# Kernel optimization log

Measured on AMD Instinct MI355X. Metric: run time of the kernel, lower is better.

## Reference

```python
import jax, jax.numpy as jnp
import numpy as np

T, TOPK = 512, 2
E, H, D = 8, 2816, 1024


def setup_inputs() -> dict:
    key = jax.random.key(0)
    k1, k2, k3, k4, k5 = jax.random.split(key, 5)
    x = jax.random.normal(k1, (T, D), dtype=jnp.float32)
    expert_indices = jax.random.randint(k2, (T, TOPK), 0, E, dtype=jnp.int64)
    w1 = jax.random.normal(k3, (E, H, D), dtype=jnp.float32)
    w2 = jax.random.normal(k4, (E, H, D), dtype=jnp.float32)
    w3 = jax.random.normal(k5, (E, H, D), dtype=jnp.float32)
    return {"x": x, "expert_indices": expert_indices, "w1": w1, "w2": w2, "w3": w3}


def reference(x, expert_indices, w1, w2, w3):
    # Math identical to: silu(x @ w1[e].T) * (x @ w3[e].T) @ w2[e] for e = expert_indices[t, a].
    # Computed densely over all experts (GEMM-friendly), then gathered per token,
    # which avoids materializing [T, a, H, D] gathered weight tensors.
    h1 = jax.nn.silu(jnp.einsum('ti,ehi->teh', x, w1))   # [T, E, H]
    h3 = jnp.einsum('ti,ehi->teh', x, w3)                # [T, E, H]
    out_all = jnp.einsum('teh,ehi->tei', h1 * h3, w2)    # [T, E, D]
    # gather the top_k selected experts per token -> [T, TOPK, D]
    idx = expert_indices[:, :, None]                     # [T, a, 1]
    expert_outs = jnp.take_along_axis(out_all, idx, axis=1)
    return expert_outs
```

## Files before the change

kernel.cpp:

```cpp
#include <hip/hip_runtime.h>


#define NEXP 8
#define HDIM 2816
#define DDIM 1024
#define NPAIR 1024

typedef unsigned int uint;
typedef unsigned short ushort;
typedef __attribute__((ext_vector_type(8))) short bf16x8;
typedef __attribute__((ext_vector_type(4))) float fvec4;
typedef __attribute__((ext_vector_type(4))) uint uvec4;
typedef __attribute__((ext_vector_type(2))) uint uvec2;

__device__ __forceinline__ ushort f2bf(float f) {
    uint u = __builtin_bit_cast(uint, f);
    u += 0x7fff + ((u >> 16) & 1);
    return (ushort)(u >> 16);
}
__device__ __forceinline__ uint pack2(float lo, float hi) {
    return (uint)f2bf(lo) | ((uint)f2bf(hi) << 16);
}

__global__ void route_kernel(const int* __restrict__ idx,
                             int* __restrict__ counts,
                             int* __restrict__ lists) {
    int p = threadIdx.x;
    if (p < NEXP) counts[p] = 0;
    __syncthreads();
    int e = idx[p];
    int pos = atomicAdd(&counts[e], 1);
    lists[e * NPAIR + pos] = p;
}

__global__ void h_mfma(const float* __restrict__ x,
                       const float* __restrict__ w1,
                       const float* __restrict__ w3,
                       const int* __restrict__ counts,
                       const int* __restrict__ lists,
                       ushort* __restrict__ hb) {
    const int e = blockIdx.x;
    const int cnt = counts[e];
    const int m0 = blockIdx.z * 128;
    if (m0 >= cnt) return;
    const int h0 = blockIdx.y * 64;

    __shared__ ushort sA[128 * 32];
    __shared__ ushort sB1[64 * 32];
    __shared__ ushort sB3[64 * 32];
    __shared__ int sTok[128];
    __shared__ int sPairS[128];

    const int tid = threadIdx.x;
    if (tid < 128) {
        int m = m0 + tid;
        int mc = (m < cnt) ? m : (cnt - 1);
        int p = lists[e * NPAIR + mc];
        sTok[tid] = p >> 1;
        sPairS[tid] = (m < cnt) ? p : -1;
    }
    __syncthreads();

    const int w = tid >> 6;
    const int lane = tid & 63;
    const int l16 = lane & 15;
    const int quad = lane >> 4;

    fvec4 acc1[2][4], acc3[2][4];
    #pragma unroll
    for (int i = 0; i < 2; ++i)
        #pragma unroll
        for (int j = 0; j < 4; ++j) { acc1[i][j] = (fvec4)0.f; acc3[i][j] = (fvec4)0.f; }

    const float* w1e = w1 + (size_t)e * HDIM * DDIM + (size_t)h0 * DDIM;
    const float* w3e = w3 + (size_t)e * HDIM * DDIM + (size_t)h0 * DDIM;

    for (int k0 = 0; k0 < DDIM; k0 += 32) {
        fvec4 va[4], vb1[2], vb3[2];
        #pragma unroll
        for (int it = 0; it < 4; ++it) {
            int ii = tid + it * 256;
            int row = ii >> 3, c4 = ii & 7;
            va[it] = *(const fvec4*)(x + (size_t)sTok[row] * DDIM + k0 + c4 * 4);
        }
        #pragma unroll
        for (int it = 0; it < 2; ++it) {
            int ii = tid + it * 256;
            int row = ii >> 3, c4 = ii & 7;
            vb1[it] = *(const fvec4*)(w1e + (size_t)row * DDIM + k0 + c4 * 4);
            vb3[it] = *(const fvec4*)(w3e + (size_t)row * DDIM + k0 + c4 * 4);
        }
        __syncthreads();
        #pragma unroll
        for (int it = 0; it < 4; ++it) {
            int ii = tid + it * 256;
            int row = ii >> 3, c4 = ii & 7;
            uvec2 t = { pack2(va[it][0], va[it][1]), pack2(va[it][2], va[it][3]) };
            *(uvec2*)&sA[row * 32 + c4 * 4] = t;
        }
        #pragma unroll
        for (int it = 0; it < 2; ++it) {
            int ii = tid + it * 256;
            int row = ii >> 3, c4 = ii & 7;
            uvec2 t1 = { pack2(vb1[it][0], vb1[it][1]), pack2(vb1[it][2], vb1[it][3]) };
            uvec2 t3 = { pack2(vb3[it][0], vb3[it][1]), pack2(vb3[it][2], vb3[it][3]) };
            *(uvec2*)&sB1[row * 32 + c4 * 4] = t1;
            *(uvec2*)&sB3[row * 32 + c4 * 4] = t3;
        }
        __syncthreads();

        bf16x8 bf1[4], bf3[4];
        #pragma unroll
        for (int ni = 0; ni < 4; ++ni) {
            bf1[ni] = *(const bf16x8*)&sB1[(ni * 16 + l16) * 32 + quad * 8];
            bf3[ni] = *(const bf16x8*)&sB3[(ni * 16 + l16) * 32 + quad * 8];
        }
        #pragma unroll
        for (int mi = 0; mi < 2; ++mi) {
            bf16x8 af = *(const bf16x8*)&sA[(w * 32 + mi * 16 + l16) * 32 + quad * 8];
            #pragma unroll
            for (int ni = 0; ni < 4; ++ni) {
                acc1[mi][ni] = __builtin_amdgcn_mfma_f32_16x16x32_bf16(af, bf1[ni], acc1[mi][ni], 0, 0, 0);
                acc3[mi][ni] = __builtin_amdgcn_mfma_f32_16x16x32_bf16(af, bf3[ni], acc3[mi][ni], 0, 0, 0);
            }
        }
    }

    #pragma unroll
    for (int mi = 0; mi < 2; ++mi)
        #pragma unroll
        for (int r = 0; r < 4; ++r) {
            int m = w * 32 + mi * 16 + quad * 4 + r;
            int p = sPairS[m];
            if (p >= 0) {
                size_t base = (size_t)p * HDIM + h0;
                #pragma unroll
                for (int ni = 0; ni < 4; ++ni) {
                    float a = acc1[mi][ni][r];
                    float g = acc3[mi][ni][r];
                    float s = a / (1.f + __expf(-a)) * g;
                    hb[base + ni * 16 + l16] = f2bf(s);
                }
            }
        }
}

__global__ void out_mfma(const float* __restrict__ w2,
                         const int* __restrict__ counts,
                         const int* __restrict__ lists,
                         const ushort* __restrict__ hb,
                         float* __restrict__ out) {
    const int e = blockIdx.x;
    const int cnt = counts[e];
    const int m0 = blockIdx.z * 128;
    if (m0 >= cnt) return;
    const int n0 = blockIdx.y * 32;

    __shared__ ushort sA[128 * 64];
    __shared__ ushort sB[32 * 64];
    __shared__ int sPairC[128];
    __shared__ int sPairS[128];

    const int tid = threadIdx.x;
    if (tid < 128) {
        int m = m0 + tid;
        int mc = (m < cnt) ? m : (cnt - 1);
        int p = lists[e * NPAIR + mc];
        sPairC[tid] = p;
        sPairS[tid] = (m < cnt) ? p : -1;
    }
    __syncthreads();

    const int w = tid >> 6;
    const int lane = tid & 63;
    const int l16 = lane & 15;
    const int quad = lane >> 4;

    fvec4 acc[2][2];
    #pragma unroll
    for (int i = 0; i < 2; ++i) { acc[i][0] = (fvec4)0.f; acc[i][1] = (fvec4)0.f; }

    const float* w2e = w2 + (size_t)e * HDIM * DDIM + n0;
    const int kp = tid >> 3;
    const int n4 = tid & 7;

    for (int k0 = 0; k0 < HDIM; k0 += 64) {
        uvec4 va[4];
        #pragma unroll
        for (int it = 0; it < 4; ++it) {
            int ii = tid + it * 256;
            int row = ii >> 3, c = ii & 7;
            va[it] = *(const uvec4*)(hb + (size_t)sPairC[row] * HDIM + k0 + c * 8);
        }
        fvec4 fa = *(const fvec4*)(w2e + (size_t)(k0 + kp * 2) * DDIM + n4 * 4);
        fvec4 fb = *(const fvec4*)(w2e + (size_t)(k0 + kp * 2 + 1) * DDIM + n4 * 4);
        __syncthreads();
        #pragma unroll
        for (int it = 0; it < 4; ++it) {
            int ii = tid + it * 256;
            int row = ii >> 3, c = ii & 7;
            *(uvec4*)&sA[row * 64 + c * 8] = va[it];
        }
        #pragma unroll
        for (int j = 0; j < 4; ++j) {
            int n = n4 * 4 + j;
            *(uint*)&sB[n * 64 + kp * 2] = pack2(fa[j], fb[j]);
        }
        __syncthreads();

        #pragma unroll
        for (int kk = 0; kk < 64; kk += 32) {
            bf16x8 bfr[2];
            #pragma unroll
            for (int ni = 0; ni < 2; ++ni)
                bfr[ni] = *(const bf16x8*)&sB[(ni * 16 + l16) * 64 + kk + quad * 8];
            #pragma unroll
            for (int mi = 0; mi < 2; ++mi) {
                bf16x8 af = *(const bf16x8*)&sA[(w * 32 + mi * 16 + l16) * 64 + kk + quad * 8];
                #pragma unroll
                for (int ni = 0; ni < 2; ++ni)
                    acc[mi][ni] = __builtin_amdgcn_mfma_f32_16x16x32_bf16(af, bfr[ni], acc[mi][ni], 0, 0, 0);
            }
        }
    }

    #pragma unroll
    for (int mi = 0; mi < 2; ++mi)
        #pragma unroll
        for (int r = 0; r < 4; ++r) {
            int m = w * 32 + mi * 16 + quad * 4 + r;
            int p = sPairS[m];
            if (p >= 0) {
                #pragma unroll
                for (int ni = 0; ni < 2; ++ni)
                    out[(size_t)p * DDIM + n0 + ni * 16 + l16] = acc[mi][ni][r];
            }
        }
}

extern "C" void kernel_launch(void* const* d_in, const int* in_sizes, int n_in,
                              void* d_out, int out_size, void* d_ws, size_t ws_size,
                              hipStream_t stream) {
    const float* x   = (const float*)d_in[0];
    const int*   idx = (const int*)d_in[1];
    const float* w1  = (const float*)d_in[2];
    const float* w2  = (const float*)d_in[3];
    const float* w3  = (const float*)d_in[4];
    float* out = (float*)d_out;

    char* ws = (char*)d_ws;
    int*    counts = (int*)ws;
    int*    lists  = (int*)(ws + 1024);
    ushort* hbuf   = (ushort*)(ws + 65536);

    route_kernel<<<1, NPAIR, 0, stream>>>(idx, counts, lists);
    h_mfma<<<dim3(NEXP, HDIM / 64, NPAIR / 128), 256, 0, stream>>>(
        x, w1, w3, counts, lists, hbuf);
    out_mfma<<<dim3(NEXP, DDIM / 32, NPAIR / 128), 256, 0, stream>>>(
        w2, counts, lists, hbuf, out);
}
```

Measured before the change: 325.3 us.

## Prefetch next K tile, pad LDS, use 512-thread blocks and split-K atomics

Both GEMM kernels now run 512 threads per block, each wave owning 16 rows, and load the next K-chunk from global memory into registers while MFMAs run on the current LDS tile. LDS rows are padded (36/68 halfwords) to reduce bank conflicts. The output GEMM widens the N tile to 64 and splits K four ways, accumulating into a zeroed output with float atomicAdd. This adds parallelism and overlap, at the cost of a memset, atomic traffic and nondeterministic summation order.

New measurement: 320.3 us. Within noise of the previous version (-1.5%).

```diff
diff --git a/kernel.cpp b/kernel.cpp
--- a/kernel.cpp
+++ b/kernel.cpp
@@ -22,9 +22,9 @@
     return (uint)f2bf(lo) | ((uint)f2bf(hi) << 16);
 }
 
-__global__ void route_kernel(const int* __restrict__ idx,
-                             int* __restrict__ counts,
-                             int* __restrict__ lists) {
+__global__ __launch_bounds__(1024) void route_kernel(const int* __restrict__ idx,
+                                                     int* __restrict__ counts,
+                                                     int* __restrict__ lists) {
     int p = threadIdx.x;
     if (p < NEXP) counts[p] = 0;
     __syncthreads();
@@ -33,7 +33,9 @@
     lists[e * NPAIR + pos] = p;
 }
 
-__global__ void h_mfma(const float* __restrict__ x,
+#define LDA1 36
+
+__global__ __launch_bounds__(512) void h_mfma(const float* __restrict__ x,
                        const float* __restrict__ w1,
                        const float* __restrict__ w3,
                        const int* __restrict__ counts,
@@ -45,9 +47,9 @@
     if (m0 >= cnt) return;
     const int h0 = blockIdx.y * 64;
 
-    __shared__ ushort sA[128 * 32];
-    __shared__ ushort sB1[64 * 32];
-    __shared__ ushort sB3[64 * 32];
+    __shared__ ushort sA[128 * LDA1];
+    __shared__ ushort sB1[64 * LDA1];
+    __shared__ ushort sB3[64 * LDA1];
     __shared__ int sTok[128];
     __shared__ int sPairS[128];
 
@@ -66,98 +68,92 @@
     const int l16 = lane & 15;
     const int quad = lane >> 4;
 
-    fvec4 acc1[2][4], acc3[2][4];
-    #pragma unroll
-    for (int i = 0; i < 2; ++i)
-        #pragma unroll
-        for (int j = 0; j < 4; ++j) { acc1[i][j] = (fvec4)0.f; acc3[i][j] = (fvec4)0.f; }
+    const int arow = tid >> 3;
+    const int ac4  = tid & 7;
+
+    fvec4 acc1[4], acc3[4];
+    #pragma unroll
+    for (int i = 0; i < 4; ++i) { acc1[i] = (fvec4)0.f; acc3[i] = (fvec4)0.f; }
 
     const float* w1e = w1 + (size_t)e * HDIM * DDIM + (size_t)h0 * DDIM;
     const float* w3e = w3 + (size_t)e * HDIM * DDIM + (size_t)h0 * DDIM;
+    const float* xr0 = x + (size_t)sTok[arow] * DDIM + ac4 * 4;
+    const float* xr1 = x + (size_t)sTok[arow + 64] * DDIM + ac4 * 4;
+    const float* wr1 = w1e + (size_t)arow * DDIM + ac4 * 4;
+    const float* wr3 = w3e + (size_t)arow * DDIM + ac4 * 4;
+
+    fvec4 va0, va1, vb1, vb3;
+    va0 = *(const fvec4*)(xr0);
+    va1 = *(const fvec4*)(xr1);
+    vb1 = *(const fvec4*)(wr1);
+    vb3 = *(const fvec4*)(wr3);
 
     for (int k0 = 0; k0 < DDIM; k0 += 32) {
-        fvec4 va[4], vb1[2], vb3[2];
-        #pragma unroll
-        for (int it = 0; it < 4; ++it) {
-            int ii = tid + it * 256;
-            int row = ii >> 3, c4 = ii & 7;
-            va[it] = *(const fvec4*)(x + (size_t)sTok[row] * DDIM + k0 + c4 * 4);
-        }
-        #pragma unroll
-        for (int it = 0; it < 2; ++it) {
-            int ii = tid + it * 256;
-            int row = ii >> 3, c4 = ii & 7;
-            vb1[it] = *(const fvec4*)(w1e + (size_t)row * DDIM + k0 + c4 * 4);
-            vb3[it] = *(const fvec4*)(w3e + (size_t)row * DDIM + k0 + c4 * 4);
-        }
-        __syncthreads();
-        #pragma unroll
-        for (int it = 0; it < 4; ++it) {
-            int ii = tid + it * 256;
-            int row = ii >> 3, c4 = ii & 7;
-            uvec2 t = { pack2(va[it][0], va[it][1]), pack2(va[it][2], va[it][3]) };
-            *(uvec2*)&sA[row * 32 + c4 * 4] = t;
-        }
-        #pragma unroll
-        for (int it = 0; it < 2; ++it) {
-            int ii = tid + it * 256;
-            int row = ii >> 3, c4 = ii & 7;
-            uvec2 t1 = { pack2(vb1[it][0], vb1[it][1]), pack2(vb1[it][2], vb1[it][3]) };
-            uvec2 t3 = { pack2(vb3[it][0], vb3[it][1]), pack2(vb3[it][2], vb3[it][3]) };
-            *(uvec2*)&sB1[row * 32 + c4 * 4] = t1;
-            *(uvec2*)&sB3[row * 32 + c4 * 4] = t3;
-        }
-        __syncthreads();
-
-        bf16x8 bf1[4], bf3[4];
+        __syncthreads();
+        {
+            uvec2 t;
+            t = (uvec2){ pack2(va0[0], va0[1]), pack2(va0[2], va0[3]) };
+            *(uvec2*)&sA[arow * LDA1 + ac4 * 4] = t;
+            t = (uvec2){ pack2(va1[0], va1[1]), pack2(va1[2], va1[3]) };
+            *(uvec2*)&sA[(arow + 64) * LDA1 + ac4 * 4] = t;
+            t = (uvec2){ pack2(vb1[0], vb1[1]), pack2(vb1[2], vb1[3]) };
+            *(uvec2*)&sB1[arow * LDA1 + ac4 * 4] = t;
+            t = (uvec2){ pack2(vb3[0], vb3[1]), pack2(vb3[2], vb3[3]) };
+            *(uvec2*)&sB3[arow * LDA1 + ac4 * 4] = t;
+        }
+        __syncthreads();
+
+        int kn = (k0 + 32 < DDIM) ? (k0 + 32) : k0;
+        va0 = *(const fvec4*)(xr0 + kn);
+        va1 = *(const fvec4*)(xr1 + kn);
+        vb1 = *(const fvec4*)(wr1 + kn);
+        vb3 = *(const fvec4*)(wr3 + kn);
+
+        bf16x8 af = *(const bf16x8*)&sA[(w * 16 + l16) * LDA1 + quad * 8];
         #pragma unroll
         for (int ni = 0; ni < 4; ++ni) {
-            bf1[ni] = *(const bf16x8*)&sB1[(ni * 16 + l16) * 32 + quad * 8];
-            bf3[ni] = *(const bf16x8*)&sB3[(ni * 16 + l16) * 32 + quad * 8];
-        }
-        #pragma unroll
-        for (int mi = 0; mi < 2; ++mi) {
-            bf16x8 af = *(const bf16x8*)&sA[(w * 32 + mi * 16 + l16) * 32 + quad * 8];
+            bf16x8 b1 = *(const bf16x8*)&sB1[(ni * 16 + l16) * LDA1 + quad * 8];
+            bf16x8 b3 = *(const bf16x8*)&sB3[(ni * 16 + l16) * LDA1 + quad * 8];
+            acc1[ni] = __builtin_amdgcn_mfma_f32_16x16x32_bf16(af, b1, acc1[ni], 0, 0, 0);
+            acc3[ni] = __builtin_amdgcn_mfma_f32_16x16x32_bf16(af, b3, acc3[ni], 0, 0, 0);
+        }
+    }
+
+    #pragma unroll
+    for (int r = 0; r < 4; ++r) {
+        int m = w * 16 + quad * 4 + r;
+        int p = sPairS[m];
+        if (p >= 0) {
+            size_t base = (size_t)p * HDIM + h0;
             #pragma unroll
             for (int ni = 0; ni < 4; ++ni) {
-                acc1[mi][ni] = __builtin_amdgcn_mfma_f32_16x16x32_bf16(af, bf1[ni], acc1[mi][ni], 0, 0, 0);
-                acc3[mi][ni] = __builtin_amdgcn_mfma_f32_16x16x32_bf16(af, bf3[ni], acc3[mi][ni], 0, 0, 0);
+                float a = acc1[ni][r];
+                float g = acc3[ni][r];
+                float s = a / (1.f + __expf(-a)) * g;
+                hb[base + ni * 16 + l16] = f2bf(s);
             }
         }
     }
-
-    #pragma unroll
-    for (int mi = 0; mi < 2; ++mi)
-        #pragma unroll
-        for (int r = 0; r < 4; ++r) {
-            int m = w * 32 + mi * 16 + quad * 4 + r;
-            int p = sPairS[m];
-            if (p >= 0) {
-                size_t base = (size_t)p * HDIM + h0;
-                #pragma unroll
-                for (int ni = 0; ni < 4; ++ni) {
-                    float a = acc1[mi][ni][r];
-                    float g = acc3[mi][ni][r];
-                    float s = a / (1.f + __expf(-a)) * g;
-                    hb[base + ni * 16 + l16] = f2bf(s);
-                }
-            }
-        }
-}
-
-__global__ void out_mfma(const float* __restrict__ w2,
+}
+
+#define LDA2 68
+
+__global__ __launch_bounds__(512) void out_mfma(const float* __restrict__ w2,
                          const int* __restrict__ counts,
                          const int* __restrict__ lists,
                          const ushort* __restrict__ hb,
                          float* __restrict__ out) {
     const int e = blockIdx.x;
     const int cnt = counts[e];
-    const int m0 = blockIdx.z * 128;
+    const int mb = blockIdx.z >> 2;
+    const int sk = blockIdx.z & 3;
+    const int m0 = mb * 128;
     if (m0 >= cnt) return;
-    const int n0 = blockIdx.y * 32;
-
-    __shared__ ushort sA[128 * 64];
-    __shared__ ushort sB[32 * 64];
+    const int n0 = blockIdx.y * 64;
+    const int kbase = sk * (HDIM / 4);
+
+    __shared__ ushort sA[128 * LDA2];
+    __shared__ ushort sB[64 * LDA2];
     __shared__ int sPairC[128];
     __shared__ int sPairS[128];
 
@@ -176,66 +172,65 @@
     const int l16 = lane & 15;
     const int quad = lane >> 4;
 
-    fvec4 acc[2][2];
-    #pragma unroll
-    for (int i = 0; i < 2; ++i) { acc[i][0] = (fvec4)0.f; acc[i][1] = (fvec4)0.f; }
+    const int arow = tid >> 3;
+    const int ac   = tid & 7;
+    const int kp   = tid >> 4;
+    const int n4   = tid & 15;
+
+    fvec4 acc[4];
+    #pragma unroll
+    for (int i = 0; i < 4; ++i) acc[i] = (fvec4)0.f;
 
     const float* w2e = w2 + (size_t)e * HDIM * DDIM + n0;
-    const int kp = tid >> 3;
-    const int n4 = tid & 7;
-
-    for (int k0 = 0; k0 < HDIM; k0 += 64) {
-        uvec4 va[4];
+    const ushort* ha0 = hb + (size_t)sPairC[arow] * HDIM + ac * 8;
+    const ushort* ha1 = hb + (size_t)sPairC[arow + 64] * HDIM + ac * 8;
+    const float* wk0 = w2e + (size_t)(kbase + 2 * kp) * DDIM + n4 * 4;
+
+    uvec4 va0, va1;
+    fvec4 fa, fb;
+    va0 = *(const uvec4*)(ha0 + kbase);
+    va1 = *(const uvec4*)(ha1 + kbase);
+    fa = *(const fvec4*)(wk0);
+    fb = *(const fvec4*)(wk0 + DDIM);
+
+    const int NCH = (HDIM / 4) / 64;
+    for (int kc = 0; kc < NCH; ++kc) {
+        __syncthreads();
+        *(uvec4*)&sA[arow * LDA2 + ac * 8] = va0;
+        *(uvec4*)&sA[(arow + 64) * LDA2 + ac * 8] = va1;
         #pragma unroll
-        for (int it = 0; it < 4; ++it) {
-            int ii = tid + it * 256;
-            int row = ii >> 3, c = ii & 7;
-            va[it] = *(const uvec4*)(hb + (size_t)sPairC[row] * HDIM + k0 + c * 8);
-        }
-        fvec4 fa = *(const fvec4*)(w2e + (size_t)(k0 + kp * 2) * DDIM + n4 * 4);
-        fvec4 fb = *(const fvec4*)(w2e + (size_t)(k0 + kp * 2 + 1) * DDIM + n4 * 4);
-        __syncthreads();
-        #pragma unroll
-        for (int it = 0; it < 4; ++it) {
-            int ii = tid + it * 256;
-            int row = ii >> 3, c = ii & 7;
-            *(uvec4*)&sA[row * 64 + c * 8] = va[it];
-        }
-        #pragma unroll
-        for (int j = 0; j < 4; ++j) {
-            int n = n4 * 4 + j;
-            *(uint*)&sB[n * 64 + kp * 2] = pack2(fa[j], fb[j]);
-        }
-        __syncthreads();
+        for (int j = 0; j < 4; ++j)
+            *(uint*)&sB[(n4 * 4 + j) * LDA2 + kp * 2] = pack2(fa[j], fb[j]);
+        __syncthreads();
+
+        int kcn = (kc + 1 < NCH) ? (kc + 1) : kc;
+        int koff = kcn * 64;
+        va0 = *(const uvec4*)(ha0 + kbase + koff);
+        va1 = *(const uvec4*)(ha1 + kbase + koff);
+        fa = *(const fvec4*)(wk0 + (size_t)koff * DDIM);
+        fb = *(const fvec4*)(wk0 + (size_t)(koff + 1) * DDIM);
 
         #pragma unroll
         for (int kk = 0; kk < 64; kk += 32) {
-            bf16x8 bfr[2];
+            bf16x8 af = *(const bf16x8*)&sA[(w * 16 + l16) * LDA2 + kk + quad * 8];
             #pragma unroll
-            for (int ni = 0; ni < 2; ++ni)
-                bfr[ni] = *(const bf16x8*)&sB[(ni * 16 + l16) * 64 + kk + quad * 8];
+            for (int ni = 0; ni < 4; ++ni) {
+                bf16x8 bf = *(const bf16x8*)&sB[(ni * 16 + l16) * LDA2 + kk + quad * 8];
+                acc[ni] = __builtin_amdgcn_mfma_f32_16x16x32_bf16(af, bf, acc[ni], 0, 0, 0);
+            }
+        }
+    }
+
+    #pragma unroll
+    for (int r = 0; r < 4; ++r) {
+        int m = w * 16 + quad * 4 + r;
+        int p = sPairS[m];
+        if (p >= 0) {
             #pragma unroll
-            for (int mi = 0; mi < 2; ++mi) {
-                bf16x8 af = *(const bf16x8*)&sA[(w * 32 + mi * 16 + l16) * 64 + kk + quad * 8];
-                #pragma unroll
-                for (int ni = 0; ni < 2; ++ni)
-                    acc[mi][ni] = __builtin_amdgcn_mfma_f32_16x16x32_bf16(af, bfr[ni], acc[mi][ni], 0, 0, 0);
-            }
-        }
-    }
-
-    #pragma unroll
-    for (int mi = 0; mi < 2; ++mi)
-        #pragma unroll
-        for (int r = 0; r < 4; ++r) {
-            int m = w * 32 + mi * 16 + quad * 4 + r;
-            int p = sPairS[m];
-            if (p >= 0) {
-                #pragma unroll
-                for (int ni = 0; ni < 2; ++ni)
-                    out[(size_t)p * DDIM + n0 + ni * 16 + l16] = acc[mi][ni][r];
-            }
-        }
+            for (int ni = 0; ni < 4; ++ni)
+                atomicAdd(&out[(size_t)p * DDIM + n0 + ni * 16 + l16], acc[ni][r]);
+        }
+    }
 }
 
 extern "C" void kernel_launch(void* const* d_in, const int* in_sizes, int n_in,
@@ -253,9 +248,10 @@
     int*    lists  = (int*)(ws + 1024);
     ushort* hbuf   = (ushort*)(ws + 65536);
 
+    hipMemsetAsync(out, 0, (size_t)out_size * sizeof(float), stream);
     route_kernel<<<1, NPAIR, 0, stream>>>(idx, counts, lists);
-    h_mfma<<<dim3(NEXP, HDIM / 64, NPAIR / 128), 256, 0, stream>>>(
+    h_mfma<<<dim3(NEXP, HDIM / 64, NPAIR / 128), 512, 0, stream>>>(
         x, w1, w3, counts, lists, hbuf);
-    out_mfma<<<dim3(NEXP, DDIM / 32, NPAIR / 128), 256, 0, stream>>>(
+    out_mfma<<<dim3(NEXP, DDIM / 64, (NPAIR / 128) * 4), 512, 0, stream>>>(
         w2, counts, lists, hbuf, out);
 }
```

## Double-buffer LDS with register prefetch, pad LDS rows, split-K the down projection

Applied to the files above, without the earlier changes.

Both GEMM kernels now use two padded LDS buffers (row stride 40) with a register prefetch of the next two K chunks, so global loads overlap MFMA work and LDS bank conflicts drop. The load mapping is changed so each thread reads contiguous 64-byte spans. The output kernel widens its N tile to 64, splits K four ways across blocks, and accumulates with float atomics into an output that is zeroed by a memset first. This raises parallelism but adds atomic traffic and a memset launch.

Result: slower. 332.1 us (+2.1%).

```diff
diff --git a/kernel.cpp b/kernel.cpp
--- a/kernel.cpp
+++ b/kernel.cpp
@@ -5,13 +5,13 @@
 #define HDIM 2816
 #define DDIM 1024
 #define NPAIR 1024
+#define LDA 40
 
 typedef unsigned int uint;
 typedef unsigned short ushort;
 typedef __attribute__((ext_vector_type(8))) short bf16x8;
 typedef __attribute__((ext_vector_type(4))) float fvec4;
 typedef __attribute__((ext_vector_type(4))) uint uvec4;
-typedef __attribute__((ext_vector_type(2))) uint uvec2;
 
 __device__ __forceinline__ ushort f2bf(float f) {
     uint u = __builtin_bit_cast(uint, f);
@@ -22,9 +22,9 @@
     return (uint)f2bf(lo) | ((uint)f2bf(hi) << 16);
 }
 
-__global__ void route_kernel(const int* __restrict__ idx,
-                             int* __restrict__ counts,
-                             int* __restrict__ lists) {
+__global__ __launch_bounds__(1024) void route_kernel(const int* __restrict__ idx,
+                                                     int* __restrict__ counts,
+                                                     int* __restrict__ lists) {
     int p = threadIdx.x;
     if (p < NEXP) counts[p] = 0;
     __syncthreads();
@@ -33,7 +33,7 @@
     lists[e * NPAIR + pos] = p;
 }
 
-__global__ void h_mfma(const float* __restrict__ x,
+__global__ __launch_bounds__(256) void h_mfma(const float* __restrict__ x,
                        const float* __restrict__ w1,
                        const float* __restrict__ w3,
                        const int* __restrict__ counts,
@@ -45,9 +45,9 @@
     if (m0 >= cnt) return;
     const int h0 = blockIdx.y * 64;
 
-    __shared__ ushort sA[128 * 32];
-    __shared__ ushort sB1[64 * 32];
-    __shared__ ushort sB3[64 * 32];
+    __shared__ ushort sA[2][128 * LDA];
+    __shared__ ushort sB1[2][64 * LDA];
+    __shared__ ushort sB3[2][64 * LDA];
     __shared__ int sTok[128];
     __shared__ int sPairS[128];
 
@@ -61,10 +61,14 @@
     }
     __syncthreads();
 
-    const int w = tid >> 6;
-    const int lane = tid & 63;
-    const int l16 = lane & 15;
-    const int quad = lane >> 4;
+    const int w = tid >> 6, lane = tid & 63;
+    const int l16 = lane & 15, quad = lane >> 4;
+    const int ar = tid >> 1, ah = tid & 1;
+    const int br = tid >> 2, bq = tid & 3;
+
+    const float* xa  = x + (size_t)sTok[ar] * DDIM + ah * 16;
+    const float* wb1 = w1 + (size_t)e * HDIM * DDIM + (size_t)(h0 + br) * DDIM + bq * 8;
+    const float* wb3 = w3 + (size_t)e * HDIM * DDIM + (size_t)(h0 + br) * DDIM + bq * 8;
 
     fvec4 acc1[2][4], acc3[2][4];
     #pragma unroll
@@ -72,58 +76,64 @@
         #pragma unroll
         for (int j = 0; j < 4; ++j) { acc1[i][j] = (fvec4)0.f; acc3[i][j] = (fvec4)0.f; }
 
-    const float* w1e = w1 + (size_t)e * HDIM * DDIM + (size_t)h0 * DDIM;
-    const float* w3e = w3 + (size_t)e * HDIM * DDIM + (size_t)h0 * DDIM;
-
-    for (int k0 = 0; k0 < DDIM; k0 += 32) {
-        fvec4 va[4], vb1[2], vb3[2];
-        #pragma unroll
-        for (int it = 0; it < 4; ++it) {
-            int ii = tid + it * 256;
-            int row = ii >> 3, c4 = ii & 7;
-            va[it] = *(const fvec4*)(x + (size_t)sTok[row] * DDIM + k0 + c4 * 4);
-        }
-        #pragma unroll
-        for (int it = 0; it < 2; ++it) {
-            int ii = tid + it * 256;
-            int row = ii >> 3, c4 = ii & 7;
-            vb1[it] = *(const fvec4*)(w1e + (size_t)row * DDIM + k0 + c4 * 4);
-            vb3[it] = *(const fvec4*)(w3e + (size_t)row * DDIM + k0 + c4 * 4);
-        }
-        __syncthreads();
-        #pragma unroll
-        for (int it = 0; it < 4; ++it) {
-            int ii = tid + it * 256;
-            int row = ii >> 3, c4 = ii & 7;
-            uvec2 t = { pack2(va[it][0], va[it][1]), pack2(va[it][2], va[it][3]) };
-            *(uvec2*)&sA[row * 32 + c4 * 4] = t;
-        }
-        #pragma unroll
-        for (int it = 0; it < 2; ++it) {
-            int ii = tid + it * 256;
-            int row = ii >> 3, c4 = ii & 7;
-            uvec2 t1 = { pack2(vb1[it][0], vb1[it][1]), pack2(vb1[it][2], vb1[it][3]) };
-            uvec2 t3 = { pack2(vb3[it][0], vb3[it][1]), pack2(vb3[it][2], vb3[it][3]) };
-            *(uvec2*)&sB1[row * 32 + c4 * 4] = t1;
-            *(uvec2*)&sB3[row * 32 + c4 * 4] = t3;
-        }
-        __syncthreads();
-
+    fvec4 ra[4], rb1[2], rb3[2];
+    fvec4 qa[4], qb1[2], qb3[2];
+
+    auto LOAD = [&](int kc, fvec4* a, fvec4* b1, fvec4* b3) {
+        int kk = kc * 32;
+        a[0] = *(const fvec4*)(xa + kk);      a[1] = *(const fvec4*)(xa + kk + 4);
+        a[2] = *(const fvec4*)(xa + kk + 8);  a[3] = *(const fvec4*)(xa + kk + 12);
+        b1[0] = *(const fvec4*)(wb1 + kk);    b1[1] = *(const fvec4*)(wb1 + kk + 4);
+        b3[0] = *(const fvec4*)(wb3 + kk);    b3[1] = *(const fvec4*)(wb3 + kk + 4);
+    };
+    auto STORE = [&](int buf, const fvec4* a, const fvec4* b1, const fvec4* b3) {
+        uvec4 t0 = { pack2(a[0][0],a[0][1]), pack2(a[0][2],a[0][3]),
+                     pack2(a[1][0],a[1][1]), pack2(a[1][2],a[1][3]) };
+        uvec4 t1 = { pack2(a[2][0],a[2][1]), pack2(a[2][2],a[2][3]),
+                     pack2(a[3][0],a[3][1]), pack2(a[3][2],a[3][3]) };
+        *(uvec4*)&sA[buf][ar * LDA + ah * 16]     = t0;
+        *(uvec4*)&sA[buf][ar * LDA + ah * 16 + 8] = t1;
+        uvec4 u1 = { pack2(b1[0][0],b1[0][1]), pack2(b1[0][2],b1[0][3]),
+                     pack2(b1[1][0],b1[1][1]), pack2(b1[1][2],b1[1][3]) };
+        uvec4 u3 = { pack2(b3[0][0],b3[0][1]), pack2(b3[0][2],b3[0][3]),
+                     pack2(b3[1][0],b3[1][1]), pack2(b3[1][2],b3[1][3]) };
+        *(uvec4*)&sB1[buf][br * LDA + bq * 8] = u1;
+        *(uvec4*)&sB3[buf][br * LDA + bq * 8] = u3;
+    };
+    auto MFMA = [&](int buf) {
         bf16x8 bf1[4], bf3[4];
         #pragma unroll
-        for (int ni = 0; ni < 4; ++ni) {
-            bf1[ni] = *(const bf16x8*)&sB1[(ni * 16 + l16) * 32 + quad * 8];
-            bf3[ni] = *(const bf16x8*)&sB3[(ni * 16 + l16) * 32 + quad * 8];
+        for (int nj = 0; nj < 4; ++nj) {
+            bf1[nj] = *(const bf16x8*)&sB1[buf][(nj * 16 + l16) * LDA + quad * 8];
+            bf3[nj] = *(const bf16x8*)&sB3[buf][(nj * 16 + l16) * LDA + quad * 8];
         }
         #pragma unroll
         for (int mi = 0; mi < 2; ++mi) {
-            bf16x8 af = *(const bf16x8*)&sA[(w * 32 + mi * 16 + l16) * 32 + quad * 8];
+            bf16x8 af = *(const bf16x8*)&sA[buf][(w * 32 + mi * 16 + l16) * LDA + quad * 8];
             #pragma unroll
-            for (int ni = 0; ni < 4; ++ni) {
-                acc1[mi][ni] = __builtin_amdgcn_mfma_f32_16x16x32_bf16(af, bf1[ni], acc1[mi][ni], 0, 0, 0);
-                acc3[mi][ni] = __builtin_amdgcn_mfma_f32_16x16x32_bf16(af, bf3[ni], acc3[mi][ni], 0, 0, 0);
+            for (int nj = 0; nj < 4; ++nj) {
+                acc1[mi][nj] = __builtin_amdgcn_mfma_f32_16x16x32_bf16(af, bf1[nj], acc1[mi][nj], 0, 0, 0);
+                acc3[mi][nj] = __builtin_amdgcn_mfma_f32_16x16x32_bf16(af, bf3[nj], acc3[mi][nj], 0, 0, 0);
             }
         }
+    };
+
+    const int NCH = DDIM / 32;
+    LOAD(0, ra, rb1, rb3);
+    STORE(0, ra, rb1, rb3);
+    LOAD(1, ra, rb1, rb3);
+    __syncthreads();
+    for (int kc = 0; kc < NCH; kc += 2) {
+        int k2 = (kc + 2 < NCH) ? kc + 2 : NCH - 1;
+        int k3 = (kc + 3 < NCH) ? kc + 3 : NCH - 1;
+        LOAD(k2, qa, qb1, qb3);
+        MFMA(0);
+        STORE(1, ra, rb1, rb3);
+        __syncthreads();
+        LOAD(k3, ra, rb1, rb3);
+        MFMA(1);
+        STORE(0, qa, qb1, qb3);
+        __syncthreads();
     }
 
     #pragma unroll
@@ -135,29 +145,32 @@
             if (p >= 0) {
                 size_t base = (size_t)p * HDIM + h0;
                 #pragma unroll
-                for (int ni = 0; ni < 4; ++ni) {
-                    float a = acc1[mi][ni][r];
-                    float g = acc3[mi][ni][r];
+                for (int nj = 0; nj < 4; ++nj) {
+                    float a = acc1[mi][nj][r];
+                    float g = acc3[mi][nj][r];
                     float s = a / (1.f + __expf(-a)) * g;
-                    hb[base + ni * 16 + l16] = f2bf(s);
+                    hb[base + nj * 16 + l16] = f2bf(s);
                 }
             }
         }
 }
 
-__global__ void out_mfma(const float* __restrict__ w2,
+__global__ __launch_bounds__(256) void out_mfma(const float* __restrict__ w2,
                          const int* __restrict__ counts,
                          const int* __restrict__ lists,
                          const ushort* __restrict__ hb,
                          float* __restrict__ out) {
     const int e = blockIdx.x;
     const int cnt = counts[e];
-    const int m0 = blockIdx.z * 128;
+    const int mb = blockIdx.z >> 2;
+    const int sk = blockIdx.z & 3;
+    const int m0 = mb * 128;
     if (m0 >= cnt) return;
-    const int n0 = blockIdx.y * 32;
-
-    __shared__ ushort sA[128 * 64];
-    __shared__ ushort sB[32 * 64];
+    const int n0 = blockIdx.y * 64;
+    const int kbase = sk * (HDIM / 4);
+
+    __shared__ ushort sA[2][128 * LDA];
+    __shared__ ushort sB[2][64 * LDA];
     __shared__ int sPairC[128];
     __shared__ int sPairS[128];
 
@@ -171,57 +184,66 @@
     }
     __syncthreads();
 
-    const int w = tid >> 6;
-    const int lane = tid & 63;
-    const int l16 = lane & 15;
-    const int quad = lane >> 4;
-
-    fvec4 acc[2][2];
-    #pragma unroll
-    for (int i = 0; i < 2; ++i) { acc[i][0] = (fvec4)0.f; acc[i][1] = (fvec4)0.f; }
-
-    const float* w2e = w2 + (size_t)e * HDIM * DDIM + n0;
-    const int kp = tid >> 3;
-    const int n4 = tid & 7;
-
-    for (int k0 = 0; k0 < HDIM; k0 += 64) {
-        uvec4 va[4];
-        #pragma unroll
-        for (int it = 0; it < 4; ++it) {
-            int ii = tid + it * 256;
-            int row = ii >> 3, c = ii & 7;
-            va[it] = *(const uvec4*)(hb + (size_t)sPairC[row] * HDIM + k0 + c * 8);
-        }
-        fvec4 fa = *(const fvec4*)(w2e + (size_t)(k0 + kp * 2) * DDIM + n4 * 4);
-        fvec4 fb = *(const fvec4*)(w2e + (size_t)(k0 + kp * 2 + 1) * DDIM + n4 * 4);
-        __syncthreads();
-        #pragma unroll
-        for (int it = 0; it < 4; ++it) {
-            int ii = tid + it * 256;
-            int row = ii >> 3, c = ii & 7;
-            *(uvec4*)&sA[row * 64 + c * 8] = va[it];
-        }
-        #pragma unroll
-        for (int j = 0; j < 4; ++j) {
-            int n = n4 * 4 + j;
-            *(uint*)&sB[n * 64 + kp * 2] = pack2(fa[j], fb[j]);
-        }
-        __syncthreads();
-
-        #pragma unroll
-        for (int kk = 0; kk < 64; kk += 32) {
-            bf16x8 bfr[2];
+    const int w = tid >> 6, lane = tid & 63;
+    const int l16 = lane & 15, quad = lane >> 4;
+    const int ar = tid >> 1, ah = tid & 1;
+    const int kp = tid & 15, n4 = tid >> 4;
+
+    const ushort* ha = hb + (size_t)sPairC[ar] * HDIM + kbase + ah * 16;
+    const float* wb = w2 + (size_t)e * HDIM * DDIM + (size_t)(kbase + 2 * kp) * DDIM + n0 + n4 * 4;
+
+    fvec4 acc[2][4];
+    #pragma unroll
+    for (int i = 0; i < 2; ++i)
+        #pragma unroll
+        for (int j = 0; j < 4; ++j) acc[i][j] = (fvec4)0.f;
+
+    uvec4 ra0, ra1; fvec4 rf0, rf1;
+    uvec4 qa0, qa1; fvec4 qf0, qf1;
+
+    auto LOAD = [&](int kc, uvec4& a0, uvec4& a1, fvec4& f0, fvec4& f1) {
+        a0 = *(const uvec4*)(ha + kc * 32);
+        a1 = *(const uvec4*)(ha + kc * 32 + 8);
+        f0 = *(const fvec4*)(wb + (size_t)kc * 32 * DDIM);
+        f1 = *(const fvec4*)(wb + (size_t)kc * 32 * DDIM + DDIM);
+    };
+    auto STORE = [&](int buf, const uvec4& a0, const uvec4& a1, const fvec4& f0, const fvec4& f1) {
+        *(uvec4*)&sA[buf][ar * LDA + ah * 16]     = a0;
+        *(uvec4*)&sA[buf][ar * LDA + ah * 16 + 8] = a1;
+        #pragma unroll
+        for (int j = 0; j < 4; ++j)
+            *(uint*)&sB[buf][(n4 * 4 + j) * LDA + kp * 2] = pack2(f0[j], f1[j]);
+    };
+    auto MFMA = [&](int buf) {
+        bf16x8 bfr[4];
+        #pragma unroll
+        for (int nj = 0; nj < 4; ++nj)
+            bfr[nj] = *(const bf16x8*)&sB[buf][(nj * 16 + l16) * LDA + quad * 8];
+        #pragma unroll
+        for (int mi = 0; mi < 2; ++mi) {
+            bf16x8 af = *(const bf16x8*)&sA[buf][(w * 32 + mi * 16 + l16) * LDA + quad * 8];
             #pragma unroll
-            for (int ni = 0; ni < 2; ++ni)
-                bfr[ni] = *(const bf16x8*)&sB[(ni * 16 + l16) * 64 + kk + quad * 8];
-            #pragma unroll
-            for (int mi = 0; mi < 2; ++mi) {
-                bf16x8 af = *(const bf16x8*)&sA[(w * 32 + mi * 16 + l16) * 64 + kk + quad * 8];
-                #pragma unroll
-                for (int ni = 0; ni < 2; ++ni)
-                    acc[mi][ni] = __builtin_amdgcn_mfma_f32_16x16x32_bf16(af, bfr[ni], acc[mi][ni], 0, 0, 0);
-            }
-        }
+            for (int nj = 0; nj < 4; ++nj)
+                acc[mi][nj] = __builtin_amdgcn_mfma_f32_16x16x32_bf16(af, bfr[nj], acc[mi][nj], 0, 0, 0);
+        }
+    };
+
+    const int NCH = (HDIM / 4) / 32;
+    LOAD(0, ra0, ra1, rf0, rf1);
+    STORE(0, ra0, ra1, rf0, rf1);
+    LOAD(1, ra0, ra1, rf0, rf1);
+    __syncthreads();
+    for (int kc = 0; kc < NCH; kc += 2) {
+        int k2 = (kc + 2 < NCH) ? kc + 2 : NCH - 1;
+        int k3 = (kc + 3 < NCH) ? kc + 3 : NCH - 1;
+        LOAD(k2, qa0, qa1, qf0, qf1);
+        MFMA(0);
+        STORE(1, ra0, ra1, rf0, rf1);
+        __syncthreads();
+        LOAD(k3, ra0, ra1, rf0, rf1);
+        MFMA(1);
+        STORE(0, qa0, qa1, qf0, qf1);
+        __syncthreads();
     }
 
     #pragma unroll
@@ -232,8 +254,8 @@
             int p = sPairS[m];
             if (p >= 0) {
                 #pragma unroll
-                for (int ni = 0; ni < 2; ++ni)
-                    out[(size_t)p * DDIM + n0 + ni * 16 + l16] = acc[mi][ni][r];
+                for (int nj = 0; nj < 4; ++nj)
+                    atomicAdd(&out[(size_t)p * DDIM + n0 + nj * 16 + l16], acc[mi][nj][r]);
             }
         }
 }
@@ -253,9 +275,10 @@
     int*    lists  = (int*)(ws + 1024);
     ushort* hbuf   = (ushort*)(ws + 65536);
 
+    (void)hipMemsetAsync(out, 0, (size_t)out_size * sizeof(float), stream);
     route_kernel<<<1, NPAIR, 0, stream>>>(idx, counts, lists);
     h_mfma<<<dim3(NEXP, HDIM / 64, NPAIR / 128), 256, 0, stream>>>(
         x, w1, w3, counts, lists, hbuf);
-    out_mfma<<<dim3(NEXP, DDIM / 32, NPAIR / 128), 256, 0, stream>>>(
+    out_mfma<<<dim3(NEXP, DDIM / 64, (NPAIR / 128) * 4), 256, 0, stream>>>(
         w2, counts, lists, hbuf, out);
 }
```
